# Kernel optimization log

Measured on AMD Instinct MI355X. Metric: run time of the kernel, lower is better.

The kernel has to match this reference:

```python
import jax, jax.numpy as jnp
import numpy as np


def setup_inputs() -> dict:
    key = jax.random.key(0)
    B, C, T = 16, 128, 8192
    x = jax.random.normal(key, (B, C, T), dtype=jnp.float32)
    return {"x": x}


def reference(x) -> jnp.ndarray:
    # x: (B, C, T) real EEG signals
    B, C, T = x.shape
    # "Analytic" signal as in the torch code: zero FFT bins >= T//2, then ifft.
    Xf = jnp.fft.fft(x, axis=-1)                       # complex64 (B, C, T)
    keep = (jnp.arange(T) < (T // 2))                  # (T,)
    Xf = jnp.where(keep, Xf, 0.0 + 0.0j)
    xa = jnp.fft.ifft(Xf, axis=-1)                     # complex analytic signal
    phase = jnp.arctan2(xa.imag, xa.real)              # == torch.angle, (B, C, T)

    # PLV_ij = |mean_t exp(i(phase_i - phase_j))|
    # Decompose: Re = mean(cos_i cos_j + sin_i sin_j), Im = mean(sin_i cos_j - cos_i sin_j)
    cos_p = jnp.cos(phase)                             # (B, C, T)
    sin_p = jnp.sin(phase)
    inv_t = jnp.float32(1.0 / T)
    re = (jnp.einsum('bct,bdt->bcd', cos_p, cos_p)
          + jnp.einsum('bct,bdt->bcd', sin_p, sin_p)) * inv_t
    im = (jnp.einsum('bct,bdt->bcd', sin_p, cos_p)
          - jnp.einsum('bct,bdt->bcd', cos_p, sin_p)) * inv_t
    plv = jnp.sqrt(re * re + im * im)                  # (B, C, C)
    return plv
```

## Files before the change

kernel.cpp:

```cpp
#include <hip/hip_runtime.h>
#include <hip/hip_fp16.h>
#include <math.h>

#define T_LEN 8192
#define CHN 128
#define BATCH 16
#define NKCHUNK 16

typedef short bf16x8 __attribute__((ext_vector_type(8)));
typedef float f32x16 __attribute__((ext_vector_type(16)));

#define SIN8 0.3826834323650898f
#define COS8 0.9238795325112868f
#define SROW 72
#define SPLANE (128 * SROW)

__device__ __forceinline__ ushort f2bf(float f) {
    unsigned u = __float_as_uint(f);
    unsigned r = (u + 0x7fffu + ((u >> 16) & 1u)) >> 16;
    return (ushort)r;
}

__device__ __forceinline__ void barrier_lds_only() {
    asm volatile("s_waitcnt lgkmcnt(0)" ::: "memory");
    __builtin_amdgcn_s_barrier();
}

__device__ __forceinline__ float2 cadd(float2 a, float2 b) { return make_float2(a.x + b.x, a.y + b.y); }
__device__ __forceinline__ float2 csub(float2 a, float2 b) { return make_float2(a.x - b.x, a.y - b.y); }
__device__ __forceinline__ float2 cmul(float2 a, float2 b) {
    return make_float2(a.x * b.x - a.y * b.y, a.x * b.y + a.y * b.x);
}

__device__ __forceinline__ void r4f(float2 x0, float2 x1, float2 x2, float2 x3,
                                    float2 wa, float2 wb, float2 wc,
                                    float2& y0, float2& y1, float2& y2, float2& y3) {
    float2 t0 = cadd(x0, x2), t1 = csub(x0, x2);
    float2 t2 = cadd(x1, x3), t3 = csub(x1, x3);
    y0 = cadd(t0, t2);
    y1 = cmul(csub(t0, t2), wb);
    y2 = cmul(make_float2(t1.x + t3.y, t1.y - t3.x), wa);
    y3 = cmul(make_float2(t1.x - t3.y, t1.y + t3.x), wc);
}

__device__ __forceinline__ void r4i(float2 x0, float2 x1, float2 x2, float2 x3,
                                    float2 wa, float2 wb, float2 wc,
                                    float2& y0, float2& y1, float2& y2, float2& y3) {
    float2 a1 = cmul(x1, wb);
    float2 a2 = cmul(x2, wa);
    float2 a3 = cmul(x3, wc);
    float2 u0 = cadd(x0, a1), u1 = csub(x0, a1);
    float2 p = cadd(a2, a3);
    float2 m = make_float2(-(a2.y - a3.y), a2.x - a3.x);
    y0 = cadd(u0, p); y2 = csub(u0, p);
    y1 = cadd(u1, m); y3 = csub(u1, m);
}

__device__ __forceinline__ void r8f(const float2* x, float sn, float cs, float2* y) {
    const float r22 = 0.70710678118654752f;
    float2 w1 = make_float2(cs, sn);
    float2 w2 = make_float2(cs * cs - sn * sn, 2.f * cs * sn);
    float2 w4 = cmul(w2, w2);
    float2 w6 = cmul(w4, w2);
    float2 u0 = cadd(x[0], x[4]), u1 = cadd(x[1], x[5]), u2 = cadd(x[2], x[6]), u3 = cadd(x[3], x[7]);
    float2 e0 = cmul(csub(x[0], x[4]), w1);
    float2 e1 = cmul(csub(x[1], x[5]), w1);
    float2 e2 = cmul(csub(x[2], x[6]), w1);
    float2 e3 = cmul(csub(x[3], x[7]), w1);
    float2 v0 = e0;
    float2 v1 = make_float2(r22 * (e1.x + e1.y), r22 * (e1.y - e1.x));
    float2 v2 = make_float2(e2.y, -e2.x);
    float2 v3 = make_float2(r22 * (e3.y - e3.x), -r22 * (e3.x + e3.y));
    r4f(u0, u1, u2, u3, w2, w4, w6, y[0], y[1], y[2], y[3]);
    r4f(v0, v1, v2, v3, w2, w4, w6, y[4], y[5], y[6], y[7]);
}

__device__ __forceinline__ void r8i(const float2* x, float sn, float cs, float2* y) {
    const float r22 = 0.70710678118654752f;
    float2 w1 = make_float2(cs, sn);
    float2 w2 = make_float2(cs * cs - sn * sn, 2.f * cs * sn);
    float2 w4 = cmul(w2, w2);
    float2 w6 = cmul(w4, w2);
    float2 g0, g1, g2, g3, g4, g5, g6, g7;
    r4i(x[0], x[1], x[2], x[3], w2, w4, w6, g0, g1, g2, g3);
    r4i(x[4], x[5], x[6], x[7], w2, w4, w6, g4, g5, g6, g7);
    float2 t0 = cmul(g4, w1);
    float2 e1 = cmul(g5, w1);
    float2 e2 = cmul(g6, w1);
    float2 e3 = cmul(g7, w1);
    float2 t1 = make_float2(r22 * (e1.x - e1.y), r22 * (e1.x + e1.y));
    float2 t2 = make_float2(-e2.y, e2.x);
    float2 t3 = make_float2(-r22 * (e3.x + e3.y), r22 * (e3.x - e3.y));
    y[0] = cadd(g0, t0); y[4] = csub(g0, t0);
    y[1] = cadd(g1, t1); y[5] = csub(g1, t1);
    y[2] = cadd(g2, t2); y[6] = csub(g2, t2);
    y[3] = cadd(g3, t3); y[7] = csub(g3, t3);
}

__global__ __launch_bounds__(512, 4) void fft_analytic_kernel(const float* __restrict__ x,
                                                              ushort* __restrict__ zc,
                                                              ushort* __restrict__ zs) {
    __shared__ __align__(16) float2 buf[T_LEN];
    const int tid = threadIdx.x;
    const int row = blockIdx.x;
    const float* xr = x + ((size_t)row << 13);

    for (int s = 0; s < 2; ++s) {
        const int g = tid + (s << 9);
        float2 X[8], Y[8];
#pragma unroll
        for (int c = 0; c < 8; ++c) X[c] = make_float2(xr[g + (c << 10)], 0.f);
        float sn, cs;
        __sincosf(-(float)M_PI / 4096.f * (float)g, &sn, &cs);
        r8f(X, sn, cs, Y);
#pragma unroll
        for (int c = 0; c < 8; ++c) buf[g + (c << 10)] = Y[c];
    }
    __syncthreads();

    {
        const float astep = -(float)M_PI / 512.f;
        for (int s = 0; s < 2; ++s) {
            const int g = tid + (s << 9);
            const int j = g & 127;
            const int i = ((g & ~127) << 3) | j;
            float2 xx[8], yy[8];
#pragma unroll
            for (int c = 0; c < 8; ++c) xx[c] = buf[i + c * 128];
            float sn, cs;
            __sincosf(astep * (float)j, &sn, &cs);
            r8f(xx, sn, cs, yy);
#pragma unroll
            for (int c = 0; c < 8; ++c) buf[i + c * 128] = yy[c];
        }
        __syncthreads();
    }

    {
        const float astep = -(float)M_PI / 64.f;
        for (int s = 0; s < 2; ++s) {
            const int g = tid + (s << 9);
            const int j = g & 15;
            const int i = ((g & ~15) << 3) | j;
            float2 xx[8], yy[8];
#pragma unroll
            for (int c = 0; c < 8; ++c) xx[c] = buf[i + c * 16];
            float sn, cs;
            __sincosf(astep * (float)j, &sn, &cs);
            r8f(xx, sn, cs, yy);
#pragma unroll
            for (int c = 0; c < 8; ++c) buf[(i + c * 16) ^ (2 * c)] = yy[c];
        }
        __syncthreads();
    }

    {
        float2 v[16];
        float4* bb = (float4*)buf;
        const int K = tid & 7;
#pragma unroll
        for (int p = 0; p < 8; ++p) {
            float4 f = bb[8 * tid + (p ^ K)];
            v[2 * p]     = make_float2(f.x, f.y);
            v[2 * p + 1] = make_float2(f.z, f.w);
        }
        float2 xe[8], xo[8], E[8], O[8], t[8];
#pragma unroll
        for (int c = 0; c < 8; ++c) { xe[c] = v[2 * c]; xo[c] = v[2 * c + 1]; }
        r8f(xe, 0.f, 1.f, E);
        r8f(xo, -SIN8, COS8, O);
#pragma unroll
        for (int c = 0; c < 8; ++c) t[c] = cadd(E[c], O[c]);
        r8i(t, 0.f, 1.f, xe);
        r8i(t, SIN8, COS8, xo);
#pragma unroll
        for (int p = 0; p < 8; ++p)
            bb[8 * tid + (p ^ K)] = make_float4(xe[p].x, xe[p].y, xo[p].x, xo[p].y);
    }
    __syncthreads();

    {
        const float astep = (float)M_PI / 64.f;
        for (int s = 0; s < 2; ++s) {
            const int g = tid + (s << 9);
            const int j = g & 15;
            const int i = ((g & ~15) << 3) | j;
            float2 xx[8], yy[8];
#pragma unroll
            for (int c = 0; c < 8; ++c) xx[c] = buf[(i + c * 16) ^ (2 * c)];
            float sn, cs;
            __sincosf(astep * (float)j, &sn, &cs);
            r8i(xx, sn, cs, yy);
#pragma unroll
            for (int c = 0; c < 8; ++c) buf[i + c * 16] = yy[c];
        }
        __syncthreads();
    }

    {
        const float astep = (float)M_PI / 512.f;
        for (int s = 0; s < 2; ++s) {
            const int g = tid + (s << 9);
            const int j = g & 127;
            const int i = ((g & ~127) << 3) | j;
            float2 xx[8], yy[8];
#pragma unroll
            for (int c = 0; c < 8; ++c) xx[c] = buf[i + c * 128];
            float sn, cs;
            __sincosf(astep * (float)j, &sn, &cs);
            r8i(xx, sn, cs, yy);
#pragma unroll
            for (int c = 0; c < 8; ++c) buf[i + c * 128] = yy[c];
        }
        __syncthreads();
    }

    ushort* zcr = zc + ((size_t)row << 13);
    ushort* zsr = zs + ((size_t)row << 13);
    for (int s = 0; s < 2; ++s) {
        const int g = tid + (s << 9);
        float2 xx[8], yy[8];
#pragma unroll
        for (int c = 0; c < 8; ++c) xx[c] = buf[g + (c << 10)];
        float sn, cs;
        __sincosf((float)M_PI / 4096.f * (float)g, &sn, &cs);
        r8i(xx, sn, cs, yy);
#pragma unroll
        for (int c = 0; c < 8; ++c) {
            float2 vv = yy[c];
            float n2 = vv.x * vv.x + vv.y * vv.y;
            float cc = 1.f, ss = 0.f;
            if (n2 > 0.f) { float inv = rsqrtf(n2); cc = vv.x * inv; ss = vv.y * inv; }
            zcr[g + (c << 10)] = f2bf(cc);
            zsr[g + (c << 10)] = f2bf(ss);
        }
    }
}

__global__ __launch_bounds__(512, 2) void gram_kernel(const ushort* __restrict__ zc,
                                                      const ushort* __restrict__ zs,
                                                      __half2* __restrict__ partial) {
    const int b = blockIdx.x, kc = blockIdx.y;
    const int tid = threadIdx.x;
    const int wave = tid >> 6;
    const int wr = wave & 3, wcol = wave >> 2;
    const int lane31 = tid & 31;
    const int half = (tid >> 5) & 1;

    __shared__ __align__(16) ushort sZ[2 * SPLANE];

    f32x16 accRe[2], accIm[2];
#pragma unroll
    for (int v = 0; v < 2; ++v)
#pragma unroll
        for (int r = 0; r < 16; ++r) { accRe[v][r] = 0.f; accIm[v][r] = 0.f; }

    const size_t base = ((size_t)b * CHN) << 13;
    const int k0 = kc << 9;

    const ushort* srcs[4];
    int ldst[4];
#pragma unroll
    for (int q = 0; q < 4; ++q) {
        int id = tid + (q << 9);
        int plane = id >> 10;
        int rid = (id >> 3) & 127;
        int ck = id & 7;
        srcs[q] = (plane ? zs : zc) + base + ((size_t)rid << 13) + (size_t)(k0 + ck * 8);
        ldst[q] = plane * SPLANE + rid * SROW + ck * 8;
    }

    uint4 pre[2][4];
#pragma unroll
    for (int q = 0; q < 4; ++q) pre[0][q] = *(const uint4*)srcs[q];
#pragma unroll
    for (int q = 0; q < 4; ++q) pre[1][q] = *(const uint4*)(srcs[q] + 64);

#pragma unroll
    for (int it = 0; it < 8; ++it) {
        barrier_lds_only();
#pragma unroll
        for (int q = 0; q < 4; ++q) *(uint4*)&sZ[ldst[q]] = pre[it & 1][q];
        if (it < 6) {
#pragma unroll
            for (int q = 0; q < 4; ++q)
                pre[it & 1][q] = *(const uint4*)(srcs[q] + (it + 2) * 64);
        }
        barrier_lds_only();
#pragma unroll
        for (int kb = 0; kb < 64; kb += 16) {
            const int aoff = (wr * 32 + lane31) * SROW + kb + half * 8;
            bf16x8 aC = *(const bf16x8*)&sZ[aoff];
            bf16x8 aS = *(const bf16x8*)&sZ[SPLANE + aoff];
            bf16x8 aCn;
#pragma unroll
            for (int r = 0; r < 8; ++r) aCn[r] = (short)(aC[r] ^ (short)0x8000);
            bf16x8 bC[2], bS[2];
#pragma unroll
            for (int v = 0; v < 2; ++v) {
                const int boff = (wcol * 64 + v * 32 + lane31) * SROW + kb + half * 8;
                bC[v] = *(const bf16x8*)&sZ[boff];
                bS[v] = *(const bf16x8*)&sZ[SPLANE + boff];
            }
            accRe[0] = __builtin_amdgcn_mfma_f32_32x32x16_bf16(aC,  bC[0], accRe[0], 0, 0, 0);
            accRe[1] = __builtin_amdgcn_mfma_f32_32x32x16_bf16(aC,  bC[1], accRe[1], 0, 0, 0);
            accIm[0] = __builtin_amdgcn_mfma_f32_32x32x16_bf16(aS,  bC[0], accIm[0], 0, 0, 0);
            accIm[1] = __builtin_amdgcn_mfma_f32_32x32x16_bf16(aS,  bC[1], accIm[1], 0, 0, 0);
            accRe[0] = __builtin_amdgcn_mfma_f32_32x32x16_bf16(aS,  bS[0], accRe[0], 0, 0, 0);
            accRe[1] = __builtin_amdgcn_mfma_f32_32x32x16_bf16(aS,  bS[1], accRe[1], 0, 0, 0);
            accIm[0] = __builtin_amdgcn_mfma_f32_32x32x16_bf16(aCn, bS[0], accIm[0], 0, 0, 0);
            accIm[1] = __builtin_amdgcn_mfma_f32_32x32x16_bf16(aCn, bS[1], accIm[1], 0, 0, 0);
        }
    }

    __half2* pb = partial + ((size_t)(kc * BATCH + b) << 14);
#pragma unroll
    for (int v = 0; v < 2; ++v)
#pragma unroll
        for (int r = 0; r < 16; ++r) {
            int rrow = (r & 3) + 8 * (r >> 2) + 4 * half;
            int i = wr * 32 + rrow;
            int j = wcol * 64 + v * 32 + lane31;
            pb[i * CHN + j] = __floats2half2_rn(accRe[v][r], accIm[v][r]);
        }
}

__global__ __launch_bounds__(256) void reduce_kernel(const __half2* __restrict__ partial,
                                                     float* __restrict__ out) {
    const size_t i = (size_t)blockIdx.x * 256 + threadIdx.x;
    const size_t n = (size_t)BATCH * CHN * CHN;
    if (i >= n) return;
    float re = 0.0f, im = 0.0f;
#pragma unroll
    for (int c = 0; c < NKCHUNK; ++c) {
        float2 p = __half22float2(partial[(size_t)c * n + i]);
        re += p.x;
        im += p.y;
    }
    out[i] = sqrtf(re * re + im * im) * (1.0f / (float)T_LEN);
}

extern "C" void kernel_launch(void* const* d_in, const int* in_sizes, int n_in,
                              void* d_out, int out_size, void* d_ws, size_t ws_size,
                              hipStream_t stream) {
    const float* x = (const float*)d_in[0];
    float* out = (float*)d_out;

    const size_t plane_elems = (size_t)BATCH * CHN * T_LEN;
    ushort* zc = (ushort*)d_ws;
    ushort* zs = zc + plane_elems;
    __half2* partial = (__half2*)((char*)d_ws + 2 * plane_elems * sizeof(ushort));

    fft_analytic_kernel<<<BATCH * CHN, 512, 0, stream>>>(x, zc, zs);

    dim3 g2(BATCH, NKCHUNK);
    gram_kernel<<<g2, 512, 0, stream>>>(zc, zs, partial);

    const int n_out = BATCH * CHN * CHN;
    reduce_kernel<<<(n_out + 255) / 256, 256, 0, stream>>>(partial, out);
}
```

Measured before the change: 177.5 us.

## Run FFT kernel with 1024 threads, one radix-8 per thread, shuffle-split middle stage

The FFT kernel now launches 1024 threads per row, so each thread handles one radix-8 butterfly per stage instead of looping twice. The middle radix-16 stage is split across thread pairs, which combine even and odd halves with __shfl_xor, and a new LDS swizzle layout is used around that stage. The aim is more parallelism per block and fewer serial loop iterations per thread. In exchange it raises register pressure under launch_bounds(1024, 8) and adds cross-lane shuffle traffic.

```diff
diff --git a/kernel.cpp b/kernel.cpp
--- a/kernel.cpp
+++ b/kernel.cpp
@@ -97,133 +97,128 @@
     y[3] = cadd(g3, t3); y[7] = csub(g3, t3);
 }
 
-__global__ __launch_bounds__(512, 4) void fft_analytic_kernel(const float* __restrict__ x,
-                                                              ushort* __restrict__ zc,
-                                                              ushort* __restrict__ zs) {
+__global__ __launch_bounds__(1024, 8) void fft_analytic_kernel(const float* __restrict__ x,
+                                                               ushort* __restrict__ zc,
+                                                               ushort* __restrict__ zs) {
     __shared__ __align__(16) float2 buf[T_LEN];
-    const int tid = threadIdx.x;
+    const int u = threadIdx.x;
     const int row = blockIdx.x;
     const float* xr = x + ((size_t)row << 13);
 
-    for (int s = 0; s < 2; ++s) {
-        const int g = tid + (s << 9);
+    {
         float2 X[8], Y[8];
 #pragma unroll
-        for (int c = 0; c < 8; ++c) X[c] = make_float2(xr[g + (c << 10)], 0.f);
-        float sn, cs;
-        __sincosf(-(float)M_PI / 4096.f * (float)g, &sn, &cs);
+        for (int c = 0; c < 8; ++c) X[c] = make_float2(xr[u + (c << 10)], 0.f);
+        float sn, cs;
+        __sincosf(-(float)M_PI / 4096.f * (float)u, &sn, &cs);
         r8f(X, sn, cs, Y);
 #pragma unroll
-        for (int c = 0; c < 8; ++c) buf[g + (c << 10)] = Y[c];
-    }
-    __syncthreads();
-
-    {
-        const float astep = -(float)M_PI / 512.f;
-        for (int s = 0; s < 2; ++s) {
-            const int g = tid + (s << 9);
-            const int j = g & 127;
-            const int i = ((g & ~127) << 3) | j;
-            float2 xx[8], yy[8];
-#pragma unroll
-            for (int c = 0; c < 8; ++c) xx[c] = buf[i + c * 128];
-            float sn, cs;
-            __sincosf(astep * (float)j, &sn, &cs);
-            r8f(xx, sn, cs, yy);
-#pragma unroll
-            for (int c = 0; c < 8; ++c) buf[i + c * 128] = yy[c];
-        }
-        __syncthreads();
-    }
-
-    {
-        const float astep = -(float)M_PI / 64.f;
-        for (int s = 0; s < 2; ++s) {
-            const int g = tid + (s << 9);
-            const int j = g & 15;
-            const int i = ((g & ~15) << 3) | j;
-            float2 xx[8], yy[8];
-#pragma unroll
-            for (int c = 0; c < 8; ++c) xx[c] = buf[i + c * 16];
-            float sn, cs;
-            __sincosf(astep * (float)j, &sn, &cs);
-            r8f(xx, sn, cs, yy);
-#pragma unroll
-            for (int c = 0; c < 8; ++c) buf[(i + c * 16) ^ (2 * c)] = yy[c];
-        }
-        __syncthreads();
-    }
-
-    {
-        float2 v[16];
+        for (int c = 0; c < 8; ++c) buf[u + (c << 10)] = Y[c];
+    }
+    __syncthreads();
+
+    {
+        const int j = u & 127;
+        const int i = ((u & ~127) << 3) | j;
+        float2 xx[8], yy[8];
+#pragma unroll
+        for (int c = 0; c < 8; ++c) xx[c] = buf[i + (c << 7)];
+        float sn, cs;
+        __sincosf(-(float)M_PI / 512.f * (float)j, &sn, &cs);
+        r8f(xx, sn, cs, yy);
+#pragma unroll
+        for (int c = 0; c < 8; ++c) buf[i + (c << 7)] = yy[c];
+    }
+    __syncthreads();
+
+    {
+        const int j = u & 15;
+        const int i = ((u & ~15) << 3) | j;
+        const int O = j & 1, q = j >> 2, h = (j >> 1) & 1;
+        const int Tb = i >> 4;
+        float2 xx[8], yy[8];
+#pragma unroll
+        for (int c = 0; c < 8; ++c) xx[c] = buf[i + (c << 4)];
+        float sn, cs;
+        __sincosf(-(float)M_PI / 64.f * (float)j, &sn, &cs);
+        r8f(xx, sn, cs, yy);
+#pragma unroll
+        for (int c = 0; c < 8; ++c) {
+            const int T = Tb + c;
+            buf[(T << 4) + (O << 3) + 2 * (q ^ (T & 3)) + h] = yy[c];
+        }
+    }
+    __syncthreads();
+
+    {
+        const int t = u >> 1, o = u & 1;
         float4* bb = (float4*)buf;
-        const int K = tid & 7;
-#pragma unroll
-        for (int p = 0; p < 8; ++p) {
-            float4 f = bb[8 * tid + (p ^ K)];
-            v[2 * p]     = make_float2(f.x, f.y);
-            v[2 * p + 1] = make_float2(f.z, f.w);
-        }
-        float2 xe[8], xo[8], E[8], O[8], t[8];
-#pragma unroll
-        for (int c = 0; c < 8; ++c) { xe[c] = v[2 * c]; xo[c] = v[2 * c + 1]; }
-        r8f(xe, 0.f, 1.f, E);
-        r8f(xo, -SIN8, COS8, O);
-#pragma unroll
-        for (int c = 0; c < 8; ++c) t[c] = cadd(E[c], O[c]);
-        r8i(t, 0.f, 1.f, xe);
-        r8i(t, SIN8, COS8, xo);
-#pragma unroll
-        for (int p = 0; p < 8; ++p)
-            bb[8 * tid + (p ^ K)] = make_float4(xe[p].x, xe[p].y, xo[p].x, xo[p].y);
-    }
-    __syncthreads();
-
-    {
-        const float astep = (float)M_PI / 64.f;
-        for (int s = 0; s < 2; ++s) {
-            const int g = tid + (s << 9);
-            const int j = g & 15;
-            const int i = ((g & ~15) << 3) | j;
-            float2 xx[8], yy[8];
-#pragma unroll
-            for (int c = 0; c < 8; ++c) xx[c] = buf[(i + c * 16) ^ (2 * c)];
-            float sn, cs;
-            __sincosf(astep * (float)j, &sn, &cs);
-            r8i(xx, sn, cs, yy);
-#pragma unroll
-            for (int c = 0; c < 8; ++c) buf[i + c * 16] = yy[c];
-        }
-        __syncthreads();
-    }
-
-    {
-        const float astep = (float)M_PI / 512.f;
-        for (int s = 0; s < 2; ++s) {
-            const int g = tid + (s << 9);
-            const int j = g & 127;
-            const int i = ((g & ~127) << 3) | j;
-            float2 xx[8], yy[8];
-#pragma unroll
-            for (int c = 0; c < 8; ++c) xx[c] = buf[i + c * 128];
-            float sn, cs;
-            __sincosf(astep * (float)j, &sn, &cs);
-            r8i(xx, sn, cs, yy);
-#pragma unroll
-            for (int c = 0; c < 8; ++c) buf[i + c * 128] = yy[c];
-        }
-        __syncthreads();
-    }
+        const int K = t & 3;
+        const int Fb = (t << 3) + (o << 2);
+        float2 z[8], y[8], tt[8];
+#pragma unroll
+        for (int q = 0; q < 4; ++q) {
+            float4 f = bb[Fb + (q ^ K)];
+            z[2 * q]     = make_float2(f.x, f.y);
+            z[2 * q + 1] = make_float2(f.z, f.w);
+        }
+        const float snf = o ? -SIN8 : 0.f;
+        const float csf = o ? COS8 : 1.f;
+        r8f(z, snf, csf, y);
+#pragma unroll
+        for (int c = 0; c < 8; ++c) {
+            tt[c].x = y[c].x + __shfl_xor(y[c].x, 1);
+            tt[c].y = y[c].y + __shfl_xor(y[c].y, 1);
+        }
+        const float sni = o ? SIN8 : 0.f;
+        r8i(tt, sni, csf, z);
+#pragma unroll
+        for (int q = 0; q < 4; ++q)
+            bb[Fb + (q ^ K)] = make_float4(z[2 * q].x, z[2 * q].y, z[2 * q + 1].x, z[2 * q + 1].y);
+    }
+    __syncthreads();
+
+    {
+        const int j = u & 15;
+        const int i = ((u & ~15) << 3) | j;
+        const int O = j & 1, q = j >> 2, h = (j >> 1) & 1;
+        const int Tb = i >> 4;
+        float2 xx[8], yy[8];
+#pragma unroll
+        for (int c = 0; c < 8; ++c) {
+            const int T = Tb + c;
+            xx[c] = buf[(T << 4) + (O << 3) + 2 * (q ^ (T & 3)) + h];
+        }
+        float sn, cs;
+        __sincosf((float)M_PI / 64.f * (float)j, &sn, &cs);
+        r8i(xx, sn, cs, yy);
+#pragma unroll
+        for (int c = 0; c < 8; ++c) buf[i + (c << 4)] = yy[c];
+    }
+    __syncthreads();
+
+    {
+        const int j = u & 127;
+        const int i = ((u & ~127) << 3) | j;
+        float2 xx[8], yy[8];
+#pragma unroll
+        for (int c = 0; c < 8; ++c) xx[c] = buf[i + (c << 7)];
+        float sn, cs;
+        __sincosf((float)M_PI / 512.f * (float)j, &sn, &cs);
+        r8i(xx, sn, cs, yy);
+#pragma unroll
+        for (int c = 0; c < 8; ++c) buf[i + (c << 7)] = yy[c];
+    }
+    __syncthreads();
 
     ushort* zcr = zc + ((size_t)row << 13);
     ushort* zsr = zs + ((size_t)row << 13);
-    for (int s = 0; s < 2; ++s) {
-        const int g = tid + (s << 9);
-        float2 xx[8], yy[8];
-#pragma unroll
-        for (int c = 0; c < 8; ++c) xx[c] = buf[g + (c << 10)];
-        float sn, cs;
-        __sincosf((float)M_PI / 4096.f * (float)g, &sn, &cs);
+    {
+        float2 xx[8], yy[8];
+#pragma unroll
+        for (int c = 0; c < 8; ++c) xx[c] = buf[u + (c << 10)];
+        float sn, cs;
+        __sincosf((float)M_PI / 4096.f * (float)u, &sn, &cs);
         r8i(xx, sn, cs, yy);
 #pragma unroll
         for (int c = 0; c < 8; ++c) {
@@ -231,8 +226,8 @@
             float n2 = vv.x * vv.x + vv.y * vv.y;
             float cc = 1.f, ss = 0.f;
             if (n2 > 0.f) { float inv = rsqrtf(n2); cc = vv.x * inv; ss = vv.y * inv; }
-            zcr[g + (c << 10)] = f2bf(cc);
-            zsr[g + (c << 10)] = f2bf(ss);
+            zcr[u + (c << 10)] = f2bf(cc);
+            zsr[u + (c << 10)] = f2bf(ss);
         }
     }
 }
@@ -351,7 +346,7 @@
     ushort* zs = zc + plane_elems;
     __half2* partial = (__half2*)((char*)d_ws + 2 * plane_elems * sizeof(ushort));
 
-    fft_analytic_kernel<<<BATCH * CHN, 512, 0, stream>>>(x, zc, zs);
+    fft_analytic_kernel<<<BATCH * CHN, 1024, 0, stream>>>(x, zc, zs);
 
     dim3 g2(BATCH, NKCHUNK);
     gram_kernel<<<g2, 512, 0, stream>>>(zc, zs, partial);
```

Result: slower. 185.4 us (+4.5%).
